# Kernel tuning notes

Measured on AMD Instinct MI355X. Metric: run time of the kernel, lower is better.

Reference implementation:

```python
import jax, jax.numpy as jnp
import numpy as np

D_MODEL = 2048
NUM_HEADS = 16
N_KV_HEADS = 4
HEAD_DIM = D_MODEL // NUM_HEADS  # 128
N_REP = NUM_HEADS // N_KV_HEADS  # 4
WINDOW = 256
ROPE_BASE = 10000.0
B, T = 2, 2048


def setup_inputs() -> dict:
    key = jax.random.key(0)
    ks = jax.random.split(key, 5)
    s_in = 1.0 / np.sqrt(D_MODEL)
    return {
        "x": jax.random.normal(ks[0], (B, T, D_MODEL), jnp.float32),
        "Wq": jax.random.normal(ks[1], (D_MODEL, D_MODEL), jnp.float32) * s_in,
        "Wk": jax.random.normal(ks[2], (D_MODEL, N_KV_HEADS * HEAD_DIM), jnp.float32) * s_in,
        "Wv": jax.random.normal(ks[3], (D_MODEL, N_KV_HEADS * HEAD_DIM), jnp.float32) * s_in,
        "Wo": jax.random.normal(ks[4], (D_MODEL, D_MODEL), jnp.float32) * s_in,
    }


def _rope_tables(seqlen, dtype):
    inv_freq = 1.0 / (ROPE_BASE ** (jnp.arange(0, HEAD_DIM, 2, dtype=jnp.float32) / HEAD_DIM))
    t = jnp.arange(seqlen, dtype=jnp.float32)
    freqs = jnp.outer(t, inv_freq)              # [T, hd/2]
    emb = jnp.concatenate([freqs, freqs], -1)   # [T, hd]
    return jnp.cos(emb).astype(dtype), jnp.sin(emb).astype(dtype)


def _rotate_half(x):
    half = x.shape[-1] // 2
    return jnp.concatenate([-x[..., half:], x[..., :half]], -1)


def reference(x, Wq, Wk, Wv, Wo):
    Bb, Tt, _ = x.shape
    q = (x @ Wq).reshape(Bb, Tt, NUM_HEADS, HEAD_DIM).transpose(0, 2, 1, 3)   # [B,H,T,hd]
    k = (x @ Wk).reshape(Bb, Tt, N_KV_HEADS, HEAD_DIM).transpose(0, 2, 1, 3)  # [B,Hkv,T,hd]
    v = (x @ Wv).reshape(Bb, Tt, N_KV_HEADS, HEAD_DIM).transpose(0, 2, 1, 3)

    cos, sin = _rope_tables(Tt, q.dtype)  # [T, hd] each, broadcast over B,H
    q = q * cos + _rotate_half(q) * sin
    k = k * cos + _rotate_half(k) * sin

    # GQA: repeat kv heads to match query heads
    k = jnp.repeat(k, N_REP, axis=1)
    v = jnp.repeat(v, N_REP, axis=1)

    # banded causal sliding-window mask: 0 <= i - j < WINDOW
    rel = jnp.arange(Tt)[:, None] - jnp.arange(Tt)[None, :]
    allowed = (rel >= 0) & (rel < WINDOW)  # [T, T]

    scale = 1.0 / np.sqrt(HEAD_DIM)
    scores = jnp.einsum('bhqd,bhkd->bhqk', q, k) * scale
    scores = jnp.where(allowed, scores, jnp.finfo(scores.dtype).min)
    probs = jax.nn.softmax(scores, axis=-1)
    y = jnp.einsum('bhqk,bhkd->bhqd', probs, v)
    y = y.transpose(0, 2, 1, 3).reshape(Bb, Tt, D_MODEL)
    return y @ Wo
```

## Files before the change

kernel.cpp:

```cpp
#include <hip/hip_runtime.h>
#include <hip/hip_bf16.h>

#define D_MODEL 2048
#define SEQ_T   2048
#define NQH     16
#define NKVH    4
#define HD      128
#define WIN     256
#define BATCH   2
#define ROWS    (BATCH * SEQ_T)
#define L2_10K  13.287712379549449f
#define GK      2048

typedef __attribute__((ext_vector_type(8))) short bf8_t;
typedef __attribute__((ext_vector_type(4))) float f4_t;

__device__ __forceinline__ float bf2f(unsigned short u) {
    union { unsigned int i; float f; } v; v.i = ((unsigned int)u) << 16; return v.f;
}
__device__ __forceinline__ unsigned short f2bf(float f) {
    union { float f; unsigned int i; } v; v.f = f;
    unsigned int x = v.i;
    unsigned int lsb = (x >> 16) & 1u;
    x += 0x7fffu + lsb;
    return (unsigned short)(x >> 16);
}

__device__ __forceinline__ void async_ld16(const unsigned short* g, unsigned short* l) {
    __builtin_amdgcn_global_load_lds(
        (const __attribute__((address_space(1))) unsigned int*)(g),
        (__attribute__((address_space(3))) unsigned int*)(l), 16, 0, 0);
}

__device__ int sniff_is_f32(const unsigned short* p) {
    int sane = 0;
    for (int i = 0; i < 64; ++i) {
        unsigned short u = p[2 * i];
        int e = (u >> 7) & 0xFF;
        sane += (e >= 100 && e <= 140) ? 1 : 0;
    }
    return sane < 32;
}

__global__ __launch_bounds__(256)
void convert_all(const float* __restrict__ x,
                 const float* __restrict__ Wq, const float* __restrict__ Wk,
                 const float* __restrict__ Wv, const float* __restrict__ Wo,
                 unsigned short* __restrict__ xb,
                 unsigned short* __restrict__ Wqkvt, unsigned short* __restrict__ Wot) {
    __shared__ unsigned short Ts[32][36];
    int id = blockIdx.x;
    const int t = threadIdx.x;
    if (id < 4096) {
        int i = (id * 256 + t) * 8;
        float4 a = *(const float4*)(x + i);
        float4 b = *(const float4*)(x + i + 4);
        ushort4 o0, o1;
        o0.x = f2bf(a.x); o0.y = f2bf(a.y); o0.z = f2bf(a.z); o0.w = f2bf(a.w);
        o1.x = f2bf(b.x); o1.y = f2bf(b.y); o1.z = f2bf(b.z); o1.w = f2bf(b.w);
        *(ushort4*)(xb + i)     = o0;
        *(ushort4*)(xb + i + 4) = o1;
        return;
    }
    id -= 4096;
    const float* W; unsigned short* Wt; int N;
    const int K = D_MODEL;
    if (id < 4096)      { W = Wq; Wt = Wqkvt;                          N = 2048; }
    else if (id < 5120) { W = Wk; Wt = Wqkvt + (size_t)2048 * D_MODEL; N = 512;  id -= 4096; }
    else if (id < 6144) { W = Wv; Wt = Wqkvt + (size_t)2560 * D_MODEL; N = 512;  id -= 5120; }
    else                { W = Wo; Wt = Wot;                            N = 2048; id -= 6144; }
    const int ntn = N >> 5;
    const int n0 = (id % ntn) * 32;
    const int k0 = (id / ntn) * 32;
    {
        int r = t >> 3, c = (t & 7) * 4;
        float4 v = *(const float4*)(W + (size_t)(k0 + r) * N + n0 + c);
        Ts[r][c + 0] = f2bf(v.x); Ts[r][c + 1] = f2bf(v.y);
        Ts[r][c + 2] = f2bf(v.z); Ts[r][c + 3] = f2bf(v.w);
    }
    __syncthreads();
    {
        int n = t >> 3, k = (t & 7) * 4;
        ushort4 o;
        o.x = Ts[k + 0][n]; o.y = Ts[k + 1][n];
        o.z = Ts[k + 2][n]; o.w = Ts[k + 3][n];
        *(ushort4*)(Wt + (size_t)(n0 + n) * K + k0 + k) = o;
    }
}

__global__ __launch_bounds__(256, 3)
void gemm128r(const unsigned short* __restrict__ A,
              const unsigned short* __restrict__ Bt,
              void* __restrict__ Cq, void* __restrict__ Ck, void* __restrict__ Cvc,
              int N, int mode) {
    __shared__ __align__(16) unsigned short Ls[3][8192];

    const int tid  = threadIdx.x;
    const int w    = tid >> 6;
    const int lane = tid & 63;
    const int quad = lane >> 4;
    const int lr   = lane & 15;
    const int wm   = w >> 1;
    const int wn   = w & 1;
    const int sl   = ((quad + (lr >> 1)) & 3) * 8;

    const int ntn = N >> 7;
    const int g   = blockIdx.x;
    const int xcd = g & 7;
    const int r   = g >> 3;
    const int bm  = (xcd & 3) * 8 + (r & 7);
    const int bn  = (xcd >> 2) * (ntn >> 1) + (r >> 3);
    const int m0  = bm * 128;
    const int n0  = bn * 128;

    const unsigned short* srcA[2];
    const unsigned short* srcB[2];
    int dchunk[2];
    #pragma unroll
    for (int l = 0; l < 2; ++l) {
        int li   = l * 256 + tid;
        int row  = li >> 2;
        int slog = ((li & 3) - ((li >> 3) & 3)) & 3;
        srcA[l]   = A  + (size_t)(m0 + row) * GK + slog * 8;
        srcB[l]   = Bt + (size_t)(n0 + row) * GK + slog * 8;
        dchunk[l] = (l * 256 + w * 64) * 8;
    }

    f4_t acc[4][4];
    #pragma unroll
    for (int i = 0; i < 4; ++i)
        #pragma unroll
        for (int j = 0; j < 4; ++j) acc[i][j] = (f4_t){0.f, 0.f, 0.f, 0.f};

#define STAGE(S, KT) do {                                           \
        const int ko_ = (KT) * 32;                                  \
        async_ld16(srcA[0] + ko_, &Ls[S][dchunk[0]]);               \
        async_ld16(srcA[1] + ko_, &Ls[S][dchunk[1]]);               \
        async_ld16(srcB[0] + ko_, &Ls[S][4096 + dchunk[0]]);        \
        async_ld16(srcB[1] + ko_, &Ls[S][4096 + dchunk[1]]);        \
    } while (0)

#define GATE(NN) asm volatile("s_waitcnt vmcnt(" #NN ")" ::: "memory")

    STAGE(0, 0); STAGE(1, 1);
    GATE(4);
    __builtin_amdgcn_s_barrier();

    int Sc = 0, Ss = 2;
    for (int t = 0; t < 64; ++t) {
        const unsigned short* LA = &Ls[Sc][0];
        const unsigned short* LB = &Ls[Sc][4096];
        bf8_t af[4], bv[4];
        #pragma unroll
        for (int mf = 0; mf < 4; ++mf)
            af[mf] = *(const bf8_t*)&LA[(wm * 64 + mf * 16 + lr) * 32 + sl];
        #pragma unroll
        for (int nf = 0; nf < 4; ++nf)
            bv[nf] = *(const bf8_t*)&LB[(wn * 16 + nf * 32 + lr) * 32 + sl];
        if (t < 62) STAGE(Ss, t + 2);
        __builtin_amdgcn_s_setprio(1);
        #pragma unroll
        for (int nf = 0; nf < 4; ++nf)
            #pragma unroll
            for (int mf = 0; mf < 4; ++mf)
                acc[mf][nf] = __builtin_amdgcn_mfma_f32_16x16x32_bf16(
                    af[mf], bv[nf], acc[mf][nf], 0, 0, 0);
        __builtin_amdgcn_s_setprio(0);
        if (t < 62)       GATE(4);
        else if (t == 62) GATE(0);
        if (t < 63) __builtin_amdgcn_s_barrier();
        Sc = (Sc == 2) ? 0 : Sc + 1;
        Ss = (Ss == 2) ? 0 : Ss + 1;
    }

#undef STAGE
#undef GATE

    if (mode == 1) {
        float* C = (float*)Cq;
        #pragma unroll
        for (int mf = 0; mf < 4; ++mf)
            #pragma unroll
            for (int nf = 0; nf < 4; ++nf) {
                int c  = n0 + wn * 16 + nf * 32 + lr;
                int rb = m0 + wm * 64 + mf * 16 + quad * 4;
                #pragma unroll
                for (int rr = 0; rr < 4; ++rr)
                    C[(size_t)(rb + rr) * N + c] = acc[mf][nf][rr];
            }
        return;
    }
    if (n0 < 2048 + 512) {
        const bool isQ = (n0 < 2048);
        unsigned short* Cb = isQ ? (unsigned short*)Cq : (unsigned short*)Ck;
        const int ldc = isQ ? D_MODEL : (NKVH * HD);
        const int cb0 = isQ ? n0 : (n0 - 2048);
        float inv[2];
        #pragma unroll
        for (int p = 0; p < 2; ++p)
            inv[p] = exp2f(-(float)(wn * 16 + p * 32 + lr) * (L2_10K / 64.0f));
        #pragma unroll
        for (int mf = 0; mf < 4; ++mf) {
            #pragma unroll
            for (int rr = 0; rr < 4; ++rr) {
                int row = m0 + wm * 64 + mf * 16 + quad * 4 + rr;
                float tp = (float)(row & (SEQ_T - 1));
                #pragma unroll
                for (int p = 0; p < 2; ++p) {
                    float sn, cs;
                    sincosf(tp * inv[p], &sn, &cs);
                    float lo = acc[mf][p][rr], hi = acc[mf][p + 2][rr];
                    size_t base = (size_t)row * ldc + cb0 + wn * 16 + p * 32 + lr;
                    Cb[base]      = f2bf(lo * cs - hi * sn);
                    Cb[base + 64] = f2bf(hi * cs + lo * sn);
                }
            }
        }
    } else {
        unsigned short* Vc = (unsigned short*)Cvc;
        #pragma unroll
        for (int mf = 0; mf < 4; ++mf)
            #pragma unroll
            for (int nf = 0; nf < 4; ++nf) {
                int n    = (n0 - 2560) + wn * 16 + nf * 32 + lr;
                int kvh2 = n >> 7, d = n & 127;
                int row0 = m0 + wm * 64 + mf * 16 + quad * 4;
                int bb   = row0 >> 11, pos = row0 & (SEQ_T - 1);
                ushort4 o;
                o.x = f2bf(acc[mf][nf][0]); o.y = f2bf(acc[mf][nf][1]);
                o.z = f2bf(acc[mf][nf][2]); o.w = f2bf(acc[mf][nf][3]);
                *(ushort4*)(Vc + (size_t)(bb * 4 + kvh2) * (SEQ_T * HD)
                              + (size_t)(pos >> 5) * 4096 + d * 32 + (pos & 31)) = o;
            }
    }
}

__global__ __launch_bounds__(256)
void gemm_dual(const void* __restrict__ A, const void* __restrict__ B,
               void* __restrict__ C, int M, int N, int Kd,
               const unsigned short* __restrict__ sniffp,
               int a_dyn, int c_dyn, int c_trans) {
    __shared__ unsigned short As[64][32];
    __shared__ unsigned short Bs[64][32];
    __shared__ int s_f32;

    const int t = threadIdx.x;
    if (t == 0) s_f32 = sniff_is_f32(sniffp);

    const int m0 = blockIdx.y * 64, n0 = blockIdx.x * 64;
    const int w = t >> 6, lane = t & 63;
    const int wm = w >> 1, wn = w & 1;
    const int quad = lane >> 4, lr = lane & 15;

    f4_t acc[2][2];
    #pragma unroll
    for (int i = 0; i < 2; ++i)
        #pragma unroll
        for (int j = 0; j < 2; ++j)
            acc[i][j] = (f4_t){0.f, 0.f, 0.f, 0.f};

    const int ar = t >> 2, ac = (t & 3) * 8;
    const int bk = t >> 3, bn = (t & 7) * 8;

    __syncthreads();
    const bool in_f32 = (s_f32 != 0);
    const bool a_f32  = in_f32 && (a_dyn != 0);
    const bool c_f32  = in_f32 && (c_dyn != 0);

    for (int k0 = 0; k0 < Kd; k0 += 32) {
        __syncthreads();
        if (a_f32) {
            const float* Af = (const float*)A;
            const float4* pa = (const float4*)(Af + (size_t)(m0 + ar) * Kd + k0 + ac);
            float4 a0 = pa[0], a1 = pa[1];
            unsigned short* d = &As[ar][ac];
            d[0] = f2bf(a0.x); d[1] = f2bf(a0.y); d[2] = f2bf(a0.z); d[3] = f2bf(a0.w);
            d[4] = f2bf(a1.x); d[5] = f2bf(a1.y); d[6] = f2bf(a1.z); d[7] = f2bf(a1.w);
        } else {
            const unsigned short* Au = (const unsigned short*)A;
            *(uint4*)(&As[ar][ac]) = *(const uint4*)(Au + (size_t)(m0 + ar) * Kd + k0 + ac);
        }
        if (in_f32) {
            const float* Bf = (const float*)B;
            const float4* pb = (const float4*)(Bf + (size_t)(k0 + bk) * N + n0 + bn);
            float4 b0 = pb[0], b1 = pb[1];
            Bs[bn + 0][bk] = f2bf(b0.x); Bs[bn + 1][bk] = f2bf(b0.y);
            Bs[bn + 2][bk] = f2bf(b0.z); Bs[bn + 3][bk] = f2bf(b0.w);
            Bs[bn + 4][bk] = f2bf(b1.x); Bs[bn + 5][bk] = f2bf(b1.y);
            Bs[bn + 6][bk] = f2bf(b1.z); Bs[bn + 7][bk] = f2bf(b1.w);
        } else {
            const unsigned short* Bu = (const unsigned short*)B;
            uint4 bv = *(const uint4*)(Bu + (size_t)(k0 + bk) * N + n0 + bn);
            union { uint4 v; unsigned short s[8]; } bu; bu.v = bv;
            #pragma unroll
            for (int j = 0; j < 8; ++j) Bs[bn + j][bk] = bu.s[j];
        }
        __syncthreads();

        bf8_t va0 = *(const bf8_t*)&As[wm * 32 + 0  + lr][quad * 8];
        bf8_t va1 = *(const bf8_t*)&As[wm * 32 + 16 + lr][quad * 8];
        bf8_t vb0 = *(const bf8_t*)&Bs[wn * 32 + 0  + lr][quad * 8];
        bf8_t vb1 = *(const bf8_t*)&Bs[wn * 32 + 16 + lr][quad * 8];

        acc[0][0] = __builtin_amdgcn_mfma_f32_16x16x32_bf16(va0, vb0, acc[0][0], 0, 0, 0);
        acc[0][1] = __builtin_amdgcn_mfma_f32_16x16x32_bf16(va0, vb1, acc[0][1], 0, 0, 0);
        acc[1][0] = __builtin_amdgcn_mfma_f32_16x16x32_bf16(va1, vb0, acc[1][0], 0, 0, 0);
        acc[1][1] = __builtin_amdgcn_mfma_f32_16x16x32_bf16(va1, vb1, acc[1][1], 0, 0, 0);
    }

    if (c_trans) {
        #pragma unroll
        for (int mi = 0; mi < 2; ++mi)
            #pragma unroll
            for (int ni = 0; ni < 2; ++ni) {
                int row0 = m0 + wm * 32 + mi * 16 + quad * 4;
                int col  = n0 + wn * 32 + ni * 16 + lr;
                int kvh2 = col >> 7, d = col & 127;
                int bb   = row0 >> 11, pos = row0 & (SEQ_T - 1);
                ushort4 v;
                v.x = f2bf(acc[mi][ni][0]); v.y = f2bf(acc[mi][ni][1]);
                v.z = f2bf(acc[mi][ni][2]); v.w = f2bf(acc[mi][ni][3]);
                *(ushort4*)((unsigned short*)C + (size_t)(bb * 4 + kvh2) * (SEQ_T * HD)
                              + (size_t)(pos >> 5) * 4096 + d * 32 + (pos & 31)) = v;
            }
    } else {
        #pragma unroll
        for (int mi = 0; mi < 2; ++mi)
            #pragma unroll
            for (int ni = 0; ni < 2; ++ni)
                #pragma unroll
                for (int r = 0; r < 4; ++r) {
                    int row = m0 + wm * 32 + mi * 16 + quad * 4 + r;
                    int col = n0 + wn * 32 + ni * 16 + lr;
                    if (c_f32) ((float*)C)[(size_t)row * N + col] = acc[mi][ni][r];
                    else ((unsigned short*)C)[(size_t)row * N + col] = f2bf(acc[mi][ni][r]);
                }
    }
}

__global__ __launch_bounds__(64)
void rope_kernel(unsigned short* __restrict__ X, int nheads) {
    const int idx = blockIdx.x;
    const int h   = idx % nheads;
    const int row = idx / nheads;
    const int tpos = row % SEQ_T;
    const int i   = threadIdx.x;

    size_t base = (size_t)row * (nheads * HD) + h * HD;
    float inv = exp2f(-(float)i * (L2_10K / 64.0f));
    float a = (float)tpos * inv;
    float s, c;
    sincosf(a, &s, &c);
    float x0 = bf2f(X[base + i]);
    float x1 = bf2f(X[base + i + 64]);
    X[base + i]      = f2bf(x0 * c - x1 * s);
    X[base + i + 64] = f2bf(x1 * c + x0 * s);
}

#define KSS 136
#define PS  72

__global__ __launch_bounds__(256)
void attn_gqa(unsigned short* __restrict__ Q,
              const unsigned short* __restrict__ K,
              const unsigned short* __restrict__ Vc) {
    __shared__ unsigned short Ks[64][KSS];
    __shared__ unsigned short Vs[8192];
    __shared__ unsigned short Pw[4][32][PS];

    const int t    = threadIdx.x;
    const int g    = blockIdx.x;
    const int xcd  = g & 7;
    const int b    = xcd >> 2;
    const int kvh  = xcd & 3;
    const int q0   = (g >> 3) * 32;
    const int w    = t >> 6;
    const int lane = t & 63;
    const int quad = lane >> 4;
    const int lr   = lane & 15;
    const int h    = kvh * 4 + w;
    const float scale = 0.08838834764831845f;

    bf8_t qf[2][4];
    #pragma unroll
    for (int mt = 0; mt < 2; ++mt) {
        const unsigned short* qrow =
            Q + (size_t)(b * SEQ_T + q0 + mt * 16 + lr) * D_MODEL + h * HD;
        #pragma unroll
        for (int kk = 0; kk < 4; ++kk)
            qf[mt][kk] = *(const bf8_t*)(qrow + kk * 32 + quad * 8);
    }

    f4_t O[2][8];
    #pragma unroll
    for (int mt = 0; mt < 2; ++mt)
        #pragma unroll
        for (int dt = 0; dt < 8; ++dt) O[mt][dt] = (f4_t){0.f, 0.f, 0.f, 0.f};
    float lpart[2][4];
    #pragma unroll
    for (int mt = 0; mt < 2; ++mt)
        #pragma unroll
        for (int r = 0; r < 4; ++r) lpart[mt][r] = 0.f;

    const size_t vbase = (size_t)(b * 4 + kvh) * (SEQ_T * HD);

    for (int j = 0; j < 5; ++j) {
        const int kb = q0 - 256 + 64 * j;
        if (kb + 63 < 0) continue;
        const bool need_mask = (j == 0) || (j == 4) || (kb < 0);

        __syncthreads();
        {
            int row = t >> 2, col = (t & 3) * 32;
            int rg = kb + row;
            rg = rg < 0 ? 0 : (rg > SEQ_T - 1 ? SEQ_T - 1 : rg);
            const unsigned short* src =
                K + (size_t)(b * SEQ_T + rg) * (NKVH * HD) + kvh * HD + col;
            #pragma unroll
            for (int i = 0; i < 4; ++i)
                *(uint4*)&Ks[row][col + 8 * i] = *(const uint4*)(src + 8 * i);
        }
        {
            int s0 = kb >> 5;        s0 = s0 < 0 ? 0 : (s0 > 63 ? 63 : s0);
            int s1 = (kb + 32) >> 5; s1 = s1 < 0 ? 0 : (s1 > 63 ? 63 : s1);
            const unsigned short* vb0 = Vc + vbase + (size_t)s0 * 4096;
            const unsigned short* vb1 = Vc + vbase + (size_t)s1 * 4096;
            #pragma unroll
            for (int i = 0; i < 2; ++i) {
                int off = (w * 2 + i) * 512;
                async_ld16(vb0 + off + lane * 8, &Vs[off]);
                async_ld16(vb1 + off + lane * 8, &Vs[4096 + off]);
            }
        }
        __syncthreads();

        f4_t s[2][4];
        #pragma unroll
        for (int mt = 0; mt < 2; ++mt)
            #pragma unroll
            for (int nt = 0; nt < 4; ++nt) s[mt][nt] = (f4_t){0.f, 0.f, 0.f, 0.f};
        #pragma unroll
        for (int nt = 0; nt < 4; ++nt) {
            #pragma unroll
            for (int kk = 0; kk < 4; ++kk) {
                bf8_t kf = *(const bf8_t*)&Ks[nt * 16 + lr][kk * 32 + quad * 8];
                s[0][nt] = __builtin_amdgcn_mfma_f32_16x16x32_bf16(qf[0][kk], kf, s[0][nt], 0, 0, 0);
                s[1][nt] = __builtin_amdgcn_mfma_f32_16x16x32_bf16(qf[1][kk], kf, s[1][nt], 0, 0, 0);
            }
        }

        #pragma unroll
        for (int mt = 0; mt < 2; ++mt) {
            #pragma unroll
            for (int r = 0; r < 4; ++r) {
                const int q = q0 + mt * 16 + quad * 4 + r;
                #pragma unroll
                for (int nt = 0; nt < 4; ++nt) {
                    float pj = __expf(s[mt][nt][r] * scale);
                    if (need_mask) {
                        int jg = kb + nt * 16 + lr;
                        bool ok = (jg >= 0) && ((unsigned)(q - jg) < (unsigned)WIN);
                        pj = ok ? pj : 0.f;
                    }
                    lpart[mt][r] += pj;
                    Pw[w][mt * 16 + quad * 4 + r][nt * 16 + lr] = f2bf(pj);
                }
            }
        }

        bf8_t pf[2][2];
        #pragma unroll
        for (int mt = 0; mt < 2; ++mt)
            #pragma unroll
            for (int kk = 0; kk < 2; ++kk)
                pf[mt][kk] = *(const bf8_t*)&Pw[w][mt * 16 + lr][kk * 32 + quad * 8];
        #pragma unroll
        for (int dt = 0; dt < 8; ++dt)
            #pragma unroll
            for (int kk = 0; kk < 2; ++kk) {
                bf8_t vf = *(const bf8_t*)&Vs[kk * 4096 + (dt * 16 + lr) * 32 + quad * 8];
                O[0][dt] = __builtin_amdgcn_mfma_f32_16x16x32_bf16(pf[0][kk], vf, O[0][dt], 0, 0, 0);
                O[1][dt] = __builtin_amdgcn_mfma_f32_16x16x32_bf16(pf[1][kk], vf, O[1][dt], 0, 0, 0);
            }
    }

    #pragma unroll
    for (int off = 1; off < 16; off <<= 1)
        #pragma unroll
        for (int mt = 0; mt < 2; ++mt)
            #pragma unroll
            for (int r = 0; r < 4; ++r)
                lpart[mt][r] += __shfl_xor(lpart[mt][r], off);

    #pragma unroll
    for (int mt = 0; mt < 2; ++mt) {
        float invl[4];
        #pragma unroll
        for (int r = 0; r < 4; ++r) invl[r] = 1.0f / lpart[mt][r];
        #pragma unroll
        for (int dt = 0; dt < 8; ++dt)
            #pragma unroll
            for (int r = 0; r < 4; ++r)
                Q[(size_t)(b * SEQ_T + q0 + mt * 16 + quad * 4 + r) * D_MODEL
                  + h * HD + dt * 16 + lr] = f2bf(O[mt][dt][r] * invl[r]);
    }
}

extern "C" void kernel_launch(void* const* d_in, const int* in_sizes, int n_in,
                              void* d_out, int out_size, void* d_ws, size_t ws_size,
                              hipStream_t stream) {
    const float* x  = (const float*)d_in[0];
    const float* Wq = (const float*)d_in[1];
    const float* Wk = (const float*)d_in[2];
    const float* Wv = (const float*)d_in[3];
    const float* Wo = (const float*)d_in[4];
    const unsigned short* sniffp = (const unsigned short*)d_in[1];

    unsigned short* Qb  = (unsigned short*)d_ws;
    unsigned short* Kb  = Qb + (size_t)ROWS * D_MODEL;
    unsigned short* Vcb = Kb + (size_t)ROWS * (NKVH * HD);
    unsigned short* Wot = Vcb + (size_t)(NKVH * HD) * ROWS;

    dim3 blk(256);

    if (ws_size >= (size_t)32 * 1024 * 1024) {
        unsigned short* xb    = (unsigned short*)d_out;
        unsigned short* Wqkvt = xb + (size_t)ROWS * D_MODEL;

        convert_all<<<dim3(14336), blk, 0, stream>>>(x, Wq, Wk, Wv, Wo, xb, Wqkvt, Wot);

        gemm128r<<<dim3(768), blk, 0, stream>>>(
            xb, Wqkvt, Qb, Kb, Vcb, D_MODEL + 2 * NKVH * HD, 3);

        attn_gqa<<<dim3(512), blk, 0, stream>>>(Qb, Kb, Vcb);

        gemm128r<<<dim3(512), blk, 0, stream>>>(
            Qb, Wot, d_out, nullptr, nullptr, D_MODEL, 1);
    } else {
        gemm_dual<<<dim3(D_MODEL / 64, ROWS / 64), blk, 0, stream>>>(
            x, Wq, Qb, ROWS, D_MODEL, D_MODEL, sniffp, 1, 0, 0);
        gemm_dual<<<dim3((NKVH * HD) / 64, ROWS / 64), blk, 0, stream>>>(
            x, Wk, Kb, ROWS, NKVH * HD, D_MODEL, sniffp, 1, 0, 0);
        gemm_dual<<<dim3((NKVH * HD) / 64, ROWS / 64), blk, 0, stream>>>(
            x, Wv, Vcb, ROWS, NKVH * HD, D_MODEL, sniffp, 1, 0, 1);
        rope_kernel<<<dim3(ROWS * NQH), dim3(64), 0, stream>>>(Qb, NQH);
        rope_kernel<<<dim3(ROWS * NKVH), dim3(64), 0, stream>>>(Kb, NKVH);
        attn_gqa<<<dim3(512), blk, 0, stream>>>(Qb, Kb, Vcb);
        gemm_dual<<<dim3(D_MODEL / 64, ROWS / 64), blk, 0, stream>>>(
            Qb, Wo, d_out, ROWS, D_MODEL, D_MODEL, sniffp, 0, 1, 0);
    }
}
```

Before: 247.9 us.

## Pipeline K/V loads in attention and add 4-stage output-projection GEMM

The attention kernel now prefetches the next K tile into registers and double-buffers V in shared memory, so global loads overlap the MFMA work. It also XOR-swizzles the K shared layout to avoid bank conflicts and skips fully-masked leading tiles via jstart. The output projection switches to a new 512-thread, 128x256-tile GEMM with a 4-stage async-load ring and explicit waitcnt gating. This adds register and shared-memory pressure and relies on hand-written vmcnt counts being exactly right.

```diff
diff --git a/kernel.cpp b/kernel.cpp
--- a/kernel.cpp
+++ b/kernel.cpp
@@ -235,6 +235,95 @@
     }
 }
 
+__global__ __launch_bounds__(512, 2)
+void gemm128(const unsigned short* __restrict__ A,
+             const unsigned short* __restrict__ Bt,
+             float* __restrict__ C, int N) {
+    __shared__ __align__(16) unsigned short Ls[4][12288];
+
+    const int tid  = threadIdx.x;
+    const int w    = tid >> 6;
+    const int lane = tid & 63;
+    const int quad = lane >> 4;
+    const int lr   = lane & 15;
+    const int wm   = w >> 2;
+    const int wn   = w & 3;
+    const int sl   = ((quad + (lr >> 1)) & 3) * 8;
+
+    const int ntn = N >> 8;
+    const int g   = blockIdx.x;
+    const int xcd = g & 7;
+    const int r   = g >> 3;
+    const int bm  = (xcd & 3) * 8 + (r & 7);
+    const int bn  = (xcd >> 2) * (ntn >> 1) + (r >> 3);
+    const int m0  = bm * 128;
+    const int n0  = bn * 256;
+
+    const int slog = ((tid & 3) - ((tid >> 3) & 3)) & 3;
+    const unsigned short* srcA0 = A  + (size_t)(m0 + (tid >> 2)) * GK + slog * 8;
+    const unsigned short* srcB0 = Bt + (size_t)(n0 + (tid >> 2)) * GK + slog * 8;
+    const unsigned short* srcB1 = Bt + (size_t)(n0 + 128 + (tid >> 2)) * GK + slog * 8;
+    const int dch = w * 512;
+
+    f4_t acc[4][4];
+    #pragma unroll
+    for (int i = 0; i < 4; ++i)
+        #pragma unroll
+        for (int j = 0; j < 4; ++j) acc[i][j] = (f4_t){0.f, 0.f, 0.f, 0.f};
+
+#define STAGEB(S, KT) do {                                          \
+        const int ko_ = (KT) * 32;                                  \
+        async_ld16(srcA0 + ko_, &Ls[S][dch]);                       \
+        async_ld16(srcB0 + ko_, &Ls[S][4096 + dch]);                \
+        async_ld16(srcB1 + ko_, &Ls[S][8192 + dch]);                \
+    } while (0)
+
+#define GATE(NN) asm volatile("s_waitcnt vmcnt(" #NN ")" ::: "memory")
+
+    STAGEB(0, 0); STAGEB(1, 1); STAGEB(2, 2);
+    GATE(6);
+    __builtin_amdgcn_s_barrier();
+
+    bf8_t af[4], bv[4];
+    for (int t = 0; t < 64; ++t) {
+        const int S = t & 3;
+        #pragma unroll
+        for (int mf = 0; mf < 4; ++mf)
+            af[mf] = *(const bf8_t*)&Ls[S][(wm * 64 + mf * 16 + lr) * 32 + sl];
+        #pragma unroll
+        for (int nf = 0; nf < 4; ++nf)
+            bv[nf] = *(const bf8_t*)&Ls[S][4096 + (wn * 16 + nf * 64 + lr) * 32 + sl];
+        if (t < 61) STAGEB((t + 3) & 3, t + 3);
+        __builtin_amdgcn_s_barrier();
+        __builtin_amdgcn_s_setprio(1);
+        #pragma unroll
+        for (int nf = 0; nf < 4; ++nf)
+            #pragma unroll
+            for (int mf = 0; mf < 4; ++mf)
+                acc[mf][nf] = __builtin_amdgcn_mfma_f32_16x16x32_bf16(
+                    af[mf], bv[nf], acc[mf][nf], 0, 0, 0);
+        __builtin_amdgcn_s_setprio(0);
+        if (t < 61)      GATE(6);
+        else if (t == 61) GATE(3);
+        else if (t == 62) GATE(0);
+        if (t < 63) __builtin_amdgcn_s_barrier();
+    }
+
+#undef STAGEB
+#undef GATE
+
+    #pragma unroll
+    for (int mf = 0; mf < 4; ++mf)
+        #pragma unroll
+        for (int nf = 0; nf < 4; ++nf) {
+            int c  = n0 + wn * 16 + nf * 64 + lr;
+            int rb = m0 + wm * 64 + mf * 16 + quad * 4;
+            #pragma unroll
+            for (int rr = 0; rr < 4; ++rr)
+                C[(size_t)(rb + rr) * N + c] = acc[mf][nf][rr];
+        }
+}
+
 __global__ __launch_bounds__(256)
 void gemm_dual(const void* __restrict__ A, const void* __restrict__ B,
                void* __restrict__ C, int M, int N, int Kd,
@@ -357,15 +446,14 @@
     X[base + i + 64] = f2bf(x1 * c + x0 * s);
 }
 
-#define KSS 136
 #define PS  72
 
 __global__ __launch_bounds__(256)
 void attn_gqa(unsigned short* __restrict__ Q,
               const unsigned short* __restrict__ K,
               const unsigned short* __restrict__ Vc) {
-    __shared__ unsigned short Ks[64][KSS];
-    __shared__ unsigned short Vs[8192];
+    __shared__ unsigned short Ks[64][128];
+    __shared__ unsigned short Vs[2][8192];
     __shared__ unsigned short Pw[4][32][PS];
 
     const int t    = threadIdx.x;
@@ -403,36 +491,68 @@
         for (int r = 0; r < 4; ++r) lpart[mt][r] = 0.f;
 
     const size_t vbase = (size_t)(b * 4 + kvh) * (SEQ_T * HD);
-
-    for (int j = 0; j < 5; ++j) {
+    const int krow = t >> 2, kcol = (t & 3) * 32;
+
+    const int jstart = (q0 >= 193) ? 0 : ((193 - q0 + 63) >> 6);
+
+    uint4 kreg[4];
+    int vb = 0;
+    {
+        const int kb = q0 - 256 + 64 * jstart;
+        int rg = kb + krow;
+        rg = rg < 0 ? 0 : (rg > SEQ_T - 1 ? SEQ_T - 1 : rg);
+        const unsigned short* src =
+            K + (size_t)(b * SEQ_T + rg) * (NKVH * HD) + kvh * HD + kcol;
+        #pragma unroll
+        for (int i = 0; i < 4; ++i) kreg[i] = *(const uint4*)(src + 8 * i);
+        int s0 = kb >> 5;        s0 = s0 < 0 ? 0 : (s0 > 63 ? 63 : s0);
+        int s1 = (kb + 32) >> 5; s1 = s1 < 0 ? 0 : (s1 > 63 ? 63 : s1);
+        const unsigned short* v0p = Vc + vbase + (size_t)s0 * 4096;
+        const unsigned short* v1p = Vc + vbase + (size_t)s1 * 4096;
+        #pragma unroll
+        for (int i = 0; i < 2; ++i) {
+            int off = (w * 2 + i) * 512;
+            async_ld16(v0p + off + lane * 8, &Vs[0][off]);
+            async_ld16(v1p + off + lane * 8, &Vs[0][4096 + off]);
+        }
+    }
+
+    for (int j = jstart; j < 5; ++j) {
         const int kb = q0 - 256 + 64 * j;
-        if (kb + 63 < 0) continue;
         const bool need_mask = (j == 0) || (j == 4) || (kb < 0);
 
-        __syncthreads();
-        {
-            int row = t >> 2, col = (t & 3) * 32;
-            int rg = kb + row;
+        __builtin_amdgcn_s_barrier();
+        __builtin_amdgcn_sched_barrier(0);
+
+        #pragma unroll
+        for (int i = 0; i < 4; ++i)
+            *(uint4*)&Ks[krow][(kcol + 8 * i) ^ ((krow & 7) << 3)] = kreg[i];
+
+        if (j < 4) {
+            const int kb2 = kb + 64;
+            int rg = kb2 + krow;
             rg = rg < 0 ? 0 : (rg > SEQ_T - 1 ? SEQ_T - 1 : rg);
             const unsigned short* src =
-                K + (size_t)(b * SEQ_T + rg) * (NKVH * HD) + kvh * HD + col;
-            #pragma unroll
-            for (int i = 0; i < 4; ++i)
-                *(uint4*)&Ks[row][col + 8 * i] = *(const uint4*)(src + 8 * i);
-        }
-        {
-            int s0 = kb >> 5;        s0 = s0 < 0 ? 0 : (s0 > 63 ? 63 : s0);
-            int s1 = (kb + 32) >> 5; s1 = s1 < 0 ? 0 : (s1 > 63 ? 63 : s1);
-            const unsigned short* vb0 = Vc + vbase + (size_t)s0 * 4096;
-            const unsigned short* vb1 = Vc + vbase + (size_t)s1 * 4096;
+                K + (size_t)(b * SEQ_T + rg) * (NKVH * HD) + kvh * HD + kcol;
+            int s0 = kb2 >> 5;        s0 = s0 < 0 ? 0 : (s0 > 63 ? 63 : s0);
+            int s1 = (kb2 + 32) >> 5; s1 = s1 < 0 ? 0 : (s1 > 63 ? 63 : s1);
+            const unsigned short* v0p = Vc + vbase + (size_t)s0 * 4096;
+            const unsigned short* v1p = Vc + vbase + (size_t)s1 * 4096;
             #pragma unroll
             for (int i = 0; i < 2; ++i) {
                 int off = (w * 2 + i) * 512;
-                async_ld16(vb0 + off + lane * 8, &Vs[off]);
-                async_ld16(vb1 + off + lane * 8, &Vs[4096 + off]);
-            }
-        }
-        __syncthreads();
+                async_ld16(v0p + off + lane * 8, &Vs[vb ^ 1][off]);
+                async_ld16(v1p + off + lane * 8, &Vs[vb ^ 1][4096 + off]);
+            }
+            #pragma unroll
+            for (int i = 0; i < 4; ++i) kreg[i] = *(const uint4*)(src + 8 * i);
+            asm volatile("s_waitcnt vmcnt(8)" ::: "memory");
+        } else {
+            asm volatile("s_waitcnt vmcnt(0)" ::: "memory");
+        }
+        asm volatile("s_waitcnt lgkmcnt(0)" ::: "memory");
+        __builtin_amdgcn_s_barrier();
+        __builtin_amdgcn_sched_barrier(0);
 
         f4_t s[2][4];
         #pragma unroll
@@ -443,7 +563,8 @@
         for (int nt = 0; nt < 4; ++nt) {
             #pragma unroll
             for (int kk = 0; kk < 4; ++kk) {
-                bf8_t kf = *(const bf8_t*)&Ks[nt * 16 + lr][kk * 32 + quad * 8];
+                bf8_t kf = *(const bf8_t*)&Ks[nt * 16 + lr]
+                    [(kk * 32 + quad * 8) ^ ((lr & 7) << 3)];
                 s[0][nt] = __builtin_amdgcn_mfma_f32_16x16x32_bf16(qf[0][kk], kf, s[0][nt], 0, 0, 0);
                 s[1][nt] = __builtin_amdgcn_mfma_f32_16x16x32_bf16(qf[1][kk], kf, s[1][nt], 0, 0, 0);
             }
@@ -478,10 +599,11 @@
         for (int dt = 0; dt < 8; ++dt)
             #pragma unroll
             for (int kk = 0; kk < 2; ++kk) {
-                bf8_t vf = *(const bf8_t*)&Vs[kk * 4096 + (dt * 16 + lr) * 32 + quad * 8];
+                bf8_t vf = *(const bf8_t*)&Vs[vb][kk * 4096 + (dt * 16 + lr) * 32 + quad * 8];
                 O[0][dt] = __builtin_amdgcn_mfma_f32_16x16x32_bf16(pf[0][kk], vf, O[0][dt], 0, 0, 0);
                 O[1][dt] = __builtin_amdgcn_mfma_f32_16x16x32_bf16(pf[1][kk], vf, O[1][dt], 0, 0, 0);
             }
+        vb ^= 1;
     }
 
     #pragma unroll
@@ -534,8 +656,7 @@
 
         attn_gqa<<<dim3(512), blk, 0, stream>>>(Qb, Kb, Vcb);
 
-        gemm128r<<<dim3(512), blk, 0, stream>>>(
-            Qb, Wot, d_out, nullptr, nullptr, D_MODEL, 1);
+        gemm128<<<dim3(256), dim3(512), 0, stream>>>(Qb, Wot, (float*)d_out, D_MODEL);
     } else {
         gemm_dual<<<dim3(D_MODEL / 64, ROWS / 64), blk, 0, stream>>>(
             x, Wq, Qb, ROWS, D_MODEL, D_MODEL, sniffp, 1, 0, 0);
```

After: 252.9 us. 1.02x slower.
